# Kernel tuning notes

Measured on AMD Instinct MI355X. Metric: run time of the kernel, lower is better.

The kernel has to match this reference:

```python
import jax, jax.numpy as jnp
import numpy as np

EPS = 1e-5


def _bn(h, gamma, beta):
    # BatchNorm1d in training mode: batch statistics over node dim
    mu = h.mean(axis=0)
    var = h.var(axis=0)
    return gamma * (h - mu) * jax.lax.rsqrt(var + EPS) + beta


def _rgcn_layer(x, src, dst, etype, W, Wloop, b, n_dst):
    # Relation-specific gather-transform-scatter (DGL RelGraphConv, sum agg,
    # self-loop + bias, no regularizer).
    x_src = x[src]                                   # [E, in] gather
    num_rels = W.shape[0]
    m = jnp.zeros((x_src.shape[0], W.shape[2]), x.dtype)
    for r in range(num_rels):                        # small fixed relation count
        m = m + jnp.where((etype == r)[:, None], x_src @ W[r], 0.0)
    agg = jax.ops.segment_sum(m, dst, num_segments=n_dst)  # scatter-add to dst
    # DGL block convention: dst nodes are the prefix of src nodes
    return agg + x[:n_dst] @ Wloop + b


def setup_inputs() -> dict:
    key = jax.random.key(0)
    ks = jax.random.split(key, 16)
    N_SRC, N_DST0, N_DST1 = 200000, 50000, 10000
    E0, E1, R, H, C = 800000, 160000, 5, 256, 153
    s = 1.0 / np.sqrt(H)
    inp = {
        "x": jax.random.normal(ks[0], (N_SRC, H), jnp.float32),
        "src0": jax.random.randint(ks[1], (E0,), 0, N_SRC, jnp.int32),
        "dst0": jax.random.randint(ks[2], (E0,), 0, N_DST0, jnp.int32),
        "etype0": jax.random.randint(ks[3], (E0,), 0, R, jnp.int32),
        "src1": jax.random.randint(ks[4], (E1,), 0, N_DST0, jnp.int32),
        "dst1": jax.random.randint(ks[5], (E1,), 0, N_DST1, jnp.int32),
        "etype1": jax.random.randint(ks[6], (E1,), 0, R, jnp.int32),
        "n_dst0": N_DST0,
        "n_dst1": N_DST1,
        "W0": jax.random.normal(ks[7], (R, H, H), jnp.float32) * s,
        "Wl0": jax.random.normal(ks[8], (H, H), jnp.float32) * s,
        "b0": jnp.zeros((H,), jnp.float32),
        "g0": jnp.ones((H,), jnp.float32),
        "be0": jnp.zeros((H,), jnp.float32),
        "W1": jax.random.normal(ks[9], (R, H, H), jnp.float32) * s,
        "Wl1": jax.random.normal(ks[10], (H, H), jnp.float32) * s,
        "b1": jnp.zeros((H,), jnp.float32),
        "g1": jnp.ones((H,), jnp.float32),
        "be1": jnp.zeros((H,), jnp.float32),
        "Wm1": jax.random.normal(ks[11], (H, H), jnp.float32) * s,
        "bm1": jnp.zeros((H,), jnp.float32),
        "gm": jnp.ones((H,), jnp.float32),
        "bem": jnp.zeros((H,), jnp.float32),
        "Wm2": jax.random.normal(ks[12], (H, C), jnp.float32) * s,
        "bm2": jnp.zeros((C,), jnp.float32),
    }
    return inp


def reference(x, src0, dst0, etype0, src1, dst1, etype1, n_dst0, n_dst1,
              W0, Wl0, b0, g0, be0, W1, Wl1, b1, g1, be1,
              Wm1, bm1, gm, bem, Wm2, bm2):
    # layer 0
    h = _rgcn_layer(x, src0, dst0, etype0, W0, Wl0, b0, n_dst0)
    h = jax.nn.elu(_bn(h, g0, be0))
    # layer 1
    h = _rgcn_layer(h, src1, dst1, etype1, W1, Wl1, b1, n_dst1)
    h = jax.nn.elu(_bn(h, g1, be1))
    # MLP head (dropout is identity in eval)
    h = jax.nn.relu(_bn(h @ Wm1 + bm1, gm, bem))
    return h @ Wm2 + bm2
```

## Files before the change

### kernel.cpp

```cpp
#include <hip/hip_runtime.h>
#include <hip/hip_bf16.h>


#define HD   256
#define EPS  1e-5f
#define NREL 5
#define ND0  50000
#define ND1  10000

typedef unsigned short ushort_t;
using f32x4  = __attribute__((ext_vector_type(4))) float;
using short8 = __attribute__((ext_vector_type(8))) short;

__device__ __forceinline__ ushort_t f2b(float f) {
    union { float f; unsigned u; } x; x.f = f;
    unsigned r = x.u + 0x7FFF + ((x.u >> 16) & 1);
    return (ushort_t)(r >> 16);
}
__device__ __forceinline__ float b2f(ushort_t h) {
    union { unsigned u; float f; } x; x.u = ((unsigned)h) << 16;
    return x.f;
}

#define GLOAD_LDS16(gp, lp)                                                     \
    __builtin_amdgcn_global_load_lds(                                           \
        (const __attribute__((address_space(1))) unsigned int*)(gp),            \
        (__attribute__((address_space(3))) unsigned int*)(lp), 16, 0, 0)

struct WconvArgs {
    const float* src[14];
    ushort_t*    dst[14];
    int          N[14];
};
__global__ void wconv_all_kernel(WconvArgs a) {
    int mat = blockIdx.x >> 8;
    int id = (blockIdx.x & 255) * 256 + threadIdx.x;
    int n = id >> 8, k = id & 255;
    int N = a.N[mat];
    float v = (n < N) ? a.src[mat][(size_t)k * N + n] : 0.f;
    a.dst[mat][id] = f2b(v);
}

__global__ void xconv_kernel(const float* __restrict__ x, ushort_t* __restrict__ xb,
                             int n4) {
    int id = blockIdx.x * 256 + threadIdx.x;
    if (id >= n4) return;
    float4 v = ((const float4*)x)[id];
    ushort4 o; o.x = f2b(v.x); o.y = f2b(v.y); o.z = f2b(v.z); o.w = f2b(v.w);
    ((ushort4*)xb)[id] = o;
}

__global__ void count2_kernel(const int* __restrict__ d0, const int* __restrict__ e0, int E0,
                              const int* __restrict__ d1, const int* __restrict__ e1, int E1,
                              int* __restrict__ cnt, int* __restrict__ pos) {
    int e = blockIdx.x * 256 + threadIdx.x;
    if (e < E0) {
        pos[e] = atomicAdd(&cnt[e0[e] * ND0 + d0[e]], 1);
    } else if (e < E0 + E1) {
        int i = e - E0;
        pos[e] = atomicAdd(&cnt[NREL * ND0 + e1[i] * ND1 + d1[i]], 1);
    }
}

__global__ void scan_block_kernel(const int* __restrict__ in, int* __restrict__ out,
                                  int* __restrict__ bsum, int nb) {
    __shared__ int ts[256];
    int tid = threadIdx.x;
    int base = blockIdx.x * 1024 + tid * 4;
    int v0 = (base + 0 < nb) ? in[base + 0] : 0;
    int v1 = (base + 1 < nb) ? in[base + 1] : 0;
    int v2 = (base + 2 < nb) ? in[base + 2] : 0;
    int v3 = (base + 3 < nb) ? in[base + 3] : 0;
    int tsum = v0 + v1 + v2 + v3;
    ts[tid] = tsum;
    __syncthreads();
    for (int d = 1; d < 256; d <<= 1) {
        int t = (tid >= d) ? ts[tid - d] : 0;
        __syncthreads();
        ts[tid] += t;
        __syncthreads();
    }
    int excl = ts[tid] - tsum;
    if (base + 0 < nb) out[base + 0] = excl;
    if (base + 1 < nb) out[base + 1] = excl + v0;
    if (base + 2 < nb) out[base + 2] = excl + v0 + v1;
    if (base + 3 < nb) out[base + 3] = excl + v0 + v1 + v2;
    if (tid == 255 && bsum) bsum[blockIdx.x] = ts[255];
}

__global__ void scan_add_kernel(int* __restrict__ out, const int* __restrict__ bsum, int nb) {
    int i = blockIdx.x * 256 + threadIdx.x;
    if (i < nb) out[i] += bsum[i >> 10];
}

__global__ void fill2_kernel(const int* __restrict__ s0, const int* __restrict__ d0,
                             const int* __restrict__ e0, int E0,
                             const int* __restrict__ s1, const int* __restrict__ d1,
                             const int* __restrict__ e1, int E1,
                             const int* __restrict__ pos, const int* __restrict__ off,
                             int* __restrict__ ssrc) {
    int e = blockIdx.x * 256 + threadIdx.x;
    if (e < E0) {
        ssrc[off[e0[e] * ND0 + d0[e]] + pos[e]] = s0[e];
    } else if (e < E0 + E1) {
        int i = e - E0;
        ssrc[off[NREL * ND0 + e1[i] * ND1 + d1[i]] + pos[e]] = s1[i];
    }
}

__device__ __forceinline__ void bnelu_acc(ushort4 v, const float4& scv, const float4& shv,
                                          float& a0, float& a1, float& a2, float& a3) {
    float f0 = fmaf(b2f(v.x), scv.x, shv.x);
    float f1 = fmaf(b2f(v.y), scv.y, shv.y);
    float f2 = fmaf(b2f(v.z), scv.z, shv.z);
    float f3 = fmaf(b2f(v.w), scv.w, shv.w);
    a0 += f0 > 0.f ? f0 : expm1f(f0);
    a1 += f1 > 0.f ? f1 : expm1f(f1);
    a2 += f2 > 0.f ? f2 : expm1f(f2);
    a3 += f3 > 0.f ? f3 : expm1f(f3);
}

__global__ void gather_kernel(const ushort_t* __restrict__ feat, const int* __restrict__ ssrc,
                              const int* __restrict__ cnt, const int* __restrict__ off,
                              int nbuckets, ushort_t* __restrict__ out,
                              const float* __restrict__ sc, const float* __restrict__ sh) {
    int wave = (blockIdx.x * 256 + threadIdx.x) >> 6;
    int lane = threadIdx.x & 63;
    if (wave >= nbuckets) return;
    int deg = cnt[wave], s = off[wave];
    float a0 = 0, a1 = 0, a2 = 0, a3 = 0;
    if (sc) {
        float4 scv = ((const float4*)sc)[lane];
        float4 shv = ((const float4*)sh)[lane];
        int j = 0;
        for (; j + 4 <= deg; j += 4) {
            int r0 = ssrc[s + j + 0], r1 = ssrc[s + j + 1];
            int r2 = ssrc[s + j + 2], r3 = ssrc[s + j + 3];
            ushort4 v0 = ((const ushort4*)(feat + (size_t)r0 * HD))[lane];
            ushort4 v1 = ((const ushort4*)(feat + (size_t)r1 * HD))[lane];
            ushort4 v2 = ((const ushort4*)(feat + (size_t)r2 * HD))[lane];
            ushort4 v3 = ((const ushort4*)(feat + (size_t)r3 * HD))[lane];
            bnelu_acc(v0, scv, shv, a0, a1, a2, a3);
            bnelu_acc(v1, scv, shv, a0, a1, a2, a3);
            bnelu_acc(v2, scv, shv, a0, a1, a2, a3);
            bnelu_acc(v3, scv, shv, a0, a1, a2, a3);
        }
        for (; j < deg; j++) {
            ushort4 v = ((const ushort4*)(feat + (size_t)ssrc[s + j] * HD))[lane];
            bnelu_acc(v, scv, shv, a0, a1, a2, a3);
        }
    } else {
        int j = 0;
        for (; j + 4 <= deg; j += 4) {
            int r0 = ssrc[s + j + 0], r1 = ssrc[s + j + 1];
            int r2 = ssrc[s + j + 2], r3 = ssrc[s + j + 3];
            ushort4 v0 = ((const ushort4*)(feat + (size_t)r0 * HD))[lane];
            ushort4 v1 = ((const ushort4*)(feat + (size_t)r1 * HD))[lane];
            ushort4 v2 = ((const ushort4*)(feat + (size_t)r2 * HD))[lane];
            ushort4 v3 = ((const ushort4*)(feat + (size_t)r3 * HD))[lane];
            a0 += b2f(v0.x) + b2f(v1.x) + b2f(v2.x) + b2f(v3.x);
            a1 += b2f(v0.y) + b2f(v1.y) + b2f(v2.y) + b2f(v3.y);
            a2 += b2f(v0.z) + b2f(v1.z) + b2f(v2.z) + b2f(v3.z);
            a3 += b2f(v0.w) + b2f(v1.w) + b2f(v2.w) + b2f(v3.w);
        }
        for (; j < deg; j++) {
            ushort4 v = ((const ushort4*)(feat + (size_t)ssrc[s + j] * HD))[lane];
            a0 += b2f(v.x); a1 += b2f(v.y); a2 += b2f(v.z); a3 += b2f(v.w);
        }
    }
    ushort4 o; o.x = f2b(a0); o.y = f2b(a1); o.z = f2b(a2); o.w = f2b(a3);
    ((ushort4*)(out + (size_t)wave * HD))[lane] = o;
}

__global__ void bnprep_kernel(const float* __restrict__ sums, const float* __restrict__ g,
                              const float* __restrict__ be, float invM,
                              float* __restrict__ sc, float* __restrict__ sh) {
    int c = threadIdx.x;
    float mu = sums[c] * invM;
    float var = sums[HD + c] * invM - mu * mu;
    float s = g[c] * rsqrtf(var + EPS);
    sc[c] = s; sh[c] = be[c] - mu * s;
}

__global__ void bnact_kernel(const ushort_t* __restrict__ in, ushort_t* __restrict__ out,
                             const float* __restrict__ sc, const float* __restrict__ sh,
                             int act, int n64) {
    int id = blockIdx.x * 256 + threadIdx.x;
    if (id >= n64) return;
    int c4 = id & 63;
    ushort4 v = ((const ushort4*)in)[id];
    float4 scv = ((const float4*)sc)[c4];
    float4 shv = ((const float4*)sh)[c4];
    float f0 = fmaf(b2f(v.x), scv.x, shv.x);
    float f1 = fmaf(b2f(v.y), scv.y, shv.y);
    float f2 = fmaf(b2f(v.z), scv.z, shv.z);
    float f3 = fmaf(b2f(v.w), scv.w, shv.w);
    if (act == 2) {
        f0 = fmaxf(f0, 0.f); f1 = fmaxf(f1, 0.f);
        f2 = fmaxf(f2, 0.f); f3 = fmaxf(f3, 0.f);
    } else {
        f0 = f0 > 0.f ? f0 : expm1f(f0);
        f1 = f1 > 0.f ? f1 : expm1f(f1);
        f2 = f2 > 0.f ? f2 : expm1f(f2);
        f3 = f3 > 0.f ? f3 : expm1f(f3);
    }
    ushort4 o; o.x = f2b(f0); o.y = f2b(f1); o.z = f2b(f2); o.w = f2b(f3);
    ((ushort4*)out)[id] = o;
}

struct Seg {
    const ushort_t* A;
    const ushort_t* B;
};
struct GemmArgs {
    Seg seg[6];
    int nseg;
    const float* bias;
    float* stats;
    ushort_t* Cb;
    float* Cf;
    int M, N;
};

__launch_bounds__(512, 2)
__global__ void gemm256_kernel(GemmArgs g) {
    __shared__ __align__(1024) ushort_t As[4][8192];
    __shared__ __align__(1024) ushort_t Bs[4][8192];
    int tid = threadIdx.x;
    int w = tid >> 6, lane = tid & 63;
    int rq = lane >> 4, ci = lane & 15;
    int wm = (w >> 2) * 128, wn = (w & 3) * 64;
    int bm = blockIdx.y * 256;
    f32x4 acc[8][4] = {};
    int NT = (g.nseg * HD) >> 5;

    auto stage = [&](int b, int t) {
        int k = t << 5;
        int si = k >> 8, kl = k & 255;
        const ushort_t* Ap = g.seg[si].A;
        const ushort_t* Bp = g.seg[si].B;
        int ft = w * 2;
        GLOAD_LDS16(Ap + (size_t)(bm + ft * 16 + ci) * HD + kl + rq * 8,
                    &As[b][ft * 512 + lane * 8]);
        GLOAD_LDS16(Ap + (size_t)(bm + ft * 16 + 16 + ci) * HD + kl + rq * 8,
                    &As[b][(ft + 1) * 512 + lane * 8]);
        GLOAD_LDS16(Bp + (size_t)(ft * 16 + ci) * HD + kl + rq * 8,
                    &Bs[b][ft * 512 + lane * 8]);
        GLOAD_LDS16(Bp + (size_t)(ft * 16 + 16 + ci) * HD + kl + rq * 8,
                    &Bs[b][(ft + 1) * 512 + lane * 8]);
    };

    stage(0, 0);
    if (NT > 1) stage(1, 1);
    if (NT > 2) stage(2, 2);
    for (int t = 0; t < NT; t++) {
        int buf = t & 3;
        int rem = NT - t;
        if (rem >= 3)      asm volatile("s_waitcnt vmcnt(8)" ::: "memory");
        else if (rem == 2) asm volatile("s_waitcnt vmcnt(4)" ::: "memory");
        else               asm volatile("s_waitcnt vmcnt(0)" ::: "memory");
        __builtin_amdgcn_s_barrier();
        if (t + 3 < NT) stage((t + 3) & 3, t + 3);
        short8 bfr[4];
#pragma unroll
        for (int ni = 0; ni < 4; ni++)
            bfr[ni] = *(const short8*)&Bs[buf][((wn >> 4) + ni) * 512 + lane * 8];
#pragma unroll
        for (int mi = 0; mi < 8; mi++) {
            short8 afr = *(const short8*)&As[buf][((wm >> 4) + mi) * 512 + lane * 8];
#pragma unroll
            for (int ni = 0; ni < 4; ni++)
                acc[mi][ni] = __builtin_amdgcn_mfma_f32_16x16x32_bf16(
                    afr, bfr[ni], acc[mi][ni], 0, 0, 0);
        }
    }

#pragma unroll
    for (int ni = 0; ni < 4; ni++) {
        int col = wn + ni * 16 + ci;
        float bv = (col < g.N) ? g.bias[col] : 0.f;
#pragma unroll
        for (int mi = 0; mi < 8; mi++)
#pragma unroll
            for (int reg = 0; reg < 4; reg++) acc[mi][ni][reg] += bv;
    }
    if (g.stats) {
#pragma unroll
        for (int ni = 0; ni < 4; ni++) {
            float s = 0.f, s2 = 0.f;
#pragma unroll
            for (int mi = 0; mi < 8; mi++)
#pragma unroll
                for (int reg = 0; reg < 4; reg++) {
                    int row = bm + wm + mi * 16 + rq * 4 + reg;
                    if (row < g.M) { float v = acc[mi][ni][reg]; s += v; s2 += v * v; }
                }
            s  += __shfl_xor(s, 16);  s  += __shfl_xor(s, 32);
            s2 += __shfl_xor(s2, 16); s2 += __shfl_xor(s2, 32);
            if (rq == 0) {
                int col = wn + ni * 16 + ci;
                atomicAdd(&g.stats[col], s);
                atomicAdd(&g.stats[HD + col], s2);
            }
        }
    }
#pragma unroll
    for (int mi = 0; mi < 8; mi++)
#pragma unroll
        for (int ni = 0; ni < 4; ni++)
#pragma unroll
            for (int reg = 0; reg < 4; reg++) {
                int row = bm + wm + mi * 16 + rq * 4 + reg;
                int col = wn + ni * 16 + ci;
                if (row < g.M && col < g.N) {
                    float v = acc[mi][ni][reg];
                    if (g.Cb) g.Cb[(size_t)row * HD + col] = f2b(v);
                    else      g.Cf[(size_t)row * g.N + col] = v;
                }
            }
}

extern "C" void kernel_launch(void* const* d_in, const int* in_sizes, int n_in,
                              void* d_out, int out_size, void* d_ws, size_t ws_size,
                              hipStream_t stream) {
    const float* x   = (const float*)d_in[0];
    const int* src0  = (const int*)d_in[1];
    const int* dst0  = (const int*)d_in[2];
    const int* et0   = (const int*)d_in[3];
    const int* src1  = (const int*)d_in[4];
    const int* dst1  = (const int*)d_in[5];
    const int* et1   = (const int*)d_in[6];
    const float* W0  = (const float*)d_in[9];
    const float* Wl0 = (const float*)d_in[10];
    const float* b0  = (const float*)d_in[11];
    const float* g0  = (const float*)d_in[12];
    const float* be0 = (const float*)d_in[13];
    const float* W1  = (const float*)d_in[14];
    const float* Wl1 = (const float*)d_in[15];
    const float* b1  = (const float*)d_in[16];
    const float* g1  = (const float*)d_in[17];
    const float* be1 = (const float*)d_in[18];
    const float* Wm1 = (const float*)d_in[19];
    const float* bm1 = (const float*)d_in[20];
    const float* gm  = (const float*)d_in[21];
    const float* bem = (const float*)d_in[22];
    const float* Wm2 = (const float*)d_in[23];
    const float* bm2 = (const float*)d_in[24];

    const int E0 = in_sizes[1];
    const int E1 = in_sizes[4];
    const int NOUT = in_sizes[24];
    const int NSRC = in_sizes[0] / HD;
    const int NBKT = NREL * ND0 + NREL * ND1;

    char* p = (char*)d_ws;
    ushort_t* Wt = (ushort_t*)p;  p += (size_t)14 * 65536 * 2;
    float* st    = (float*)p;     p += 1536 * 4;
    float* bnp   = (float*)p;     p += 6 * 256 * 4;
    int* cnt     = (int*)p;       p += (size_t)NBKT * 4;
    int* off     = (int*)p;       p += (size_t)NBKT * 4;
    int* bsum    = (int*)p;       p += 1024 * 4;
    int* pos     = (int*)p;       p += (size_t)(E0 + E1) * 4;
    int* ssrc    = (int*)p;       p += (size_t)(E0 + E1) * 4;
    ushort_t* xb  = (ushort_t*)p; p += (size_t)NSRC * HD * 2;
    ushort_t* S0  = (ushort_t*)p; p += (size_t)(NREL * ND0 + 512) * HD * 2;
    ushort_t* S1  = (ushort_t*)p; p += (size_t)(NREL * ND1 + 512) * HD * 2;
    ushort_t* h0b = (ushort_t*)p; p += (size_t)(ND0 + 512) * HD * 2;
    ushort_t* h1b = (ushort_t*)p; p += (size_t)(ND1 + 512) * HD * 2;
    ushort_t* mb  = (ushort_t*)p; p += (size_t)(ND1 + 512) * HD * 2;
    ushort_t* h0a = (ushort_t*)p; p += (size_t)(ND1 + 512) * HD * 2;
    ushort_t* h1a = (ushort_t*)p; p += (size_t)(ND1 + 512) * HD * 2;
    ushort_t* ma  = (ushort_t*)p; p += (size_t)(ND1 + 512) * HD * 2;

    float* st0 = st, *st1 = st + 512, *stm = st + 1024;
    float* sc0 = bnp, *sh0 = bnp + 256, *sc1 = bnp + 512, *sh1 = bnp + 768;
    float* scm = bnp + 1024, *shm = bnp + 1280;

    ushort_t* W0t  = Wt;
    ushort_t* Wl0t = Wt + 5 * 65536;
    ushort_t* W1t  = Wt + 6 * 65536;
    ushort_t* Wl1t = Wt + 11 * 65536;
    ushort_t* Wm1t = Wt + 12 * 65536;
    ushort_t* Wm2t = Wt + 13 * 65536;

    {
        WconvArgs wa;
        for (int r = 0; r < NREL; r++) { wa.src[r] = W0 + (size_t)r * 65536; wa.dst[r] = W0t + (size_t)r * 65536; wa.N[r] = 256; }
        wa.src[5] = Wl0; wa.dst[5] = Wl0t; wa.N[5] = 256;
        for (int r = 0; r < NREL; r++) { wa.src[6 + r] = W1 + (size_t)r * 65536; wa.dst[6 + r] = W1t + (size_t)r * 65536; wa.N[6 + r] = 256; }
        wa.src[11] = Wl1; wa.dst[11] = Wl1t; wa.N[11] = 256;
        wa.src[12] = Wm1; wa.dst[12] = Wm1t; wa.N[12] = 256;
        wa.src[13] = Wm2; wa.dst[13] = Wm2t; wa.N[13] = NOUT;
        wconv_all_kernel<<<14 * 256, 256, 0, stream>>>(wa);
    }
    xconv_kernel<<<(NSRC * 64 + 255) / 256, 256, 0, stream>>>(x, xb, NSRC * 64);
    hipMemsetAsync(st, 0, 1536 * sizeof(float), stream);
    hipMemsetAsync(cnt, 0, (size_t)NBKT * sizeof(int), stream);

    int ET = E0 + E1;
    count2_kernel<<<(ET + 255) / 256, 256, 0, stream>>>(dst0, et0, E0, dst1, et1, E1, cnt, pos);
    int nsb = (NBKT + 1023) / 1024;
    scan_block_kernel<<<nsb, 256, 0, stream>>>(cnt, off, bsum, NBKT);
    scan_block_kernel<<<1, 256, 0, stream>>>(bsum, bsum, nullptr, nsb);
    scan_add_kernel<<<(NBKT + 255) / 256, 256, 0, stream>>>(off, bsum, NBKT);
    fill2_kernel<<<(ET + 255) / 256, 256, 0, stream>>>(src0, dst0, et0, E0, src1, dst1, et1, E1, pos, off, ssrc);

    gather_kernel<<<(NREL * ND0 * 64) / 256, 256, 0, stream>>>(
        xb, ssrc, cnt, off, NREL * ND0, S0, nullptr, nullptr);
    {
        GemmArgs ga = {};
        for (int s = 0; s < NREL; s++)
            ga.seg[s] = { S0 + (size_t)s * ND0 * HD, W0t + (size_t)s * 65536 };
        ga.seg[5] = { xb, Wl0t };
        ga.nseg = 6; ga.bias = b0; ga.stats = st0;
        ga.Cb = h0b; ga.Cf = nullptr; ga.M = ND0; ga.N = HD;
        gemm256_kernel<<<dim3(1, (ND0 + 255) / 256), 512, 0, stream>>>(ga);
    }
    bnprep_kernel<<<1, 256, 0, stream>>>(st0, g0, be0, 1.f / ND0, sc0, sh0);

    bnact_kernel<<<((ND1 + 240) * 64 + 255) / 256, 256, 0, stream>>>(
        h0b, h0a, sc0, sh0, 1, (ND1 + 240) * 64);
    gather_kernel<<<(NREL * ND1 * 64) / 256, 256, 0, stream>>>(
        h0b, ssrc, cnt + NREL * ND0, off + NREL * ND0, NREL * ND1, S1, sc0, sh0);
    {
        GemmArgs ga = {};
        for (int s = 0; s < NREL; s++)
            ga.seg[s] = { S1 + (size_t)s * ND1 * HD, W1t + (size_t)s * 65536 };
        ga.seg[5] = { h0a, Wl1t };
        ga.nseg = 6; ga.bias = b1; ga.stats = st1;
        ga.Cb = h1b; ga.Cf = nullptr; ga.M = ND1; ga.N = HD;
        gemm256_kernel<<<dim3(1, (ND1 + 255) / 256), 512, 0, stream>>>(ga);
    }
    bnprep_kernel<<<1, 256, 0, stream>>>(st1, g1, be1, 1.f / ND1, sc1, sh1);

    bnact_kernel<<<((ND1 + 240) * 64 + 255) / 256, 256, 0, stream>>>(
        h1b, h1a, sc1, sh1, 1, (ND1 + 240) * 64);
    {
        GemmArgs ga = {};
        ga.seg[0] = { h1a, Wm1t };
        ga.nseg = 1; ga.bias = bm1; ga.stats = stm;
        ga.Cb = mb; ga.Cf = nullptr; ga.M = ND1; ga.N = HD;
        gemm256_kernel<<<dim3(1, (ND1 + 255) / 256), 512, 0, stream>>>(ga);
    }
    bnprep_kernel<<<1, 256, 0, stream>>>(stm, gm, bem, 1.f / ND1, scm, shm);
    bnact_kernel<<<((ND1 + 240) * 64 + 255) / 256, 256, 0, stream>>>(
        mb, ma, scm, shm, 2, (ND1 + 240) * 64);
    {
        GemmArgs ga = {};
        ga.seg[0] = { ma, Wm2t };
        ga.nseg = 1; ga.bias = bm2; ga.stats = nullptr;
        ga.Cb = nullptr; ga.Cf = (float*)d_out; ga.M = ND1; ga.N = NOUT;
        gemm256_kernel<<<dim3(1, (ND1 + 255) / 256), 512, 0, stream>>>(ga);
    }
}
```

Measured before the change: 808.4 us.

## Switch GEMM to 128x128 tiles with 256 threads and simplify gather unrolling

Replaces the 256x256, 512-thread GEMM with a 128x128, 256-thread tile that also splits N across blockIdx.x. The grid therefore has more blocks to spread across the CUs, and each wave holds fewer accumulators. The gather kernel loses its 4-way unroll: the BN+ELU path now processes one neighbor per iteration and the plain path processes two, which cuts register use but reduces memory-level parallelism. Padding for bnact is enlarged to cover 128-row tiles.

```diff
diff --git a/kernel.cpp b/kernel.cpp
--- a/kernel.cpp
+++ b/kernel.cpp
@@ -108,18 +108,6 @@
     }
 }
 
-__device__ __forceinline__ void bnelu_acc(ushort4 v, const float4& scv, const float4& shv,
-                                          float& a0, float& a1, float& a2, float& a3) {
-    float f0 = fmaf(b2f(v.x), scv.x, shv.x);
-    float f1 = fmaf(b2f(v.y), scv.y, shv.y);
-    float f2 = fmaf(b2f(v.z), scv.z, shv.z);
-    float f3 = fmaf(b2f(v.w), scv.w, shv.w);
-    a0 += f0 > 0.f ? f0 : expm1f(f0);
-    a1 += f1 > 0.f ? f1 : expm1f(f1);
-    a2 += f2 > 0.f ? f2 : expm1f(f2);
-    a3 += f3 > 0.f ? f3 : expm1f(f3);
-}
-
 __global__ void gather_kernel(const ushort_t* __restrict__ feat, const int* __restrict__ ssrc,
                               const int* __restrict__ cnt, const int* __restrict__ off,
                               int nbuckets, ushort_t* __restrict__ out,
@@ -128,42 +116,31 @@
     int lane = threadIdx.x & 63;
     if (wave >= nbuckets) return;
     int deg = cnt[wave], s = off[wave];
+    float4 scv = {0, 0, 0, 0}, shv = {0, 0, 0, 0};
+    if (sc) { scv = ((const float4*)sc)[lane]; shv = ((const float4*)sh)[lane]; }
     float a0 = 0, a1 = 0, a2 = 0, a3 = 0;
     if (sc) {
-        float4 scv = ((const float4*)sc)[lane];
-        float4 shv = ((const float4*)sh)[lane];
-        int j = 0;
-        for (; j + 4 <= deg; j += 4) {
-            int r0 = ssrc[s + j + 0], r1 = ssrc[s + j + 1];
-            int r2 = ssrc[s + j + 2], r3 = ssrc[s + j + 3];
-            ushort4 v0 = ((const ushort4*)(feat + (size_t)r0 * HD))[lane];
-            ushort4 v1 = ((const ushort4*)(feat + (size_t)r1 * HD))[lane];
-            ushort4 v2 = ((const ushort4*)(feat + (size_t)r2 * HD))[lane];
-            ushort4 v3 = ((const ushort4*)(feat + (size_t)r3 * HD))[lane];
-            bnelu_acc(v0, scv, shv, a0, a1, a2, a3);
-            bnelu_acc(v1, scv, shv, a0, a1, a2, a3);
-            bnelu_acc(v2, scv, shv, a0, a1, a2, a3);
-            bnelu_acc(v3, scv, shv, a0, a1, a2, a3);
-        }
-        for (; j < deg; j++) {
+        for (int j = 0; j < deg; j++) {
             ushort4 v = ((const ushort4*)(feat + (size_t)ssrc[s + j] * HD))[lane];
-            bnelu_acc(v, scv, shv, a0, a1, a2, a3);
+            float f0 = fmaf(b2f(v.x), scv.x, shv.x);
+            float f1 = fmaf(b2f(v.y), scv.y, shv.y);
+            float f2 = fmaf(b2f(v.z), scv.z, shv.z);
+            float f3 = fmaf(b2f(v.w), scv.w, shv.w);
+            a0 += f0 > 0.f ? f0 : expm1f(f0);
+            a1 += f1 > 0.f ? f1 : expm1f(f1);
+            a2 += f2 > 0.f ? f2 : expm1f(f2);
+            a3 += f3 > 0.f ? f3 : expm1f(f3);
         }
     } else {
         int j = 0;
-        for (; j + 4 <= deg; j += 4) {
-            int r0 = ssrc[s + j + 0], r1 = ssrc[s + j + 1];
-            int r2 = ssrc[s + j + 2], r3 = ssrc[s + j + 3];
+        for (; j + 2 <= deg; j += 2) {
+            int r0 = ssrc[s + j], r1 = ssrc[s + j + 1];
             ushort4 v0 = ((const ushort4*)(feat + (size_t)r0 * HD))[lane];
             ushort4 v1 = ((const ushort4*)(feat + (size_t)r1 * HD))[lane];
-            ushort4 v2 = ((const ushort4*)(feat + (size_t)r2 * HD))[lane];
-            ushort4 v3 = ((const ushort4*)(feat + (size_t)r3 * HD))[lane];
-            a0 += b2f(v0.x) + b2f(v1.x) + b2f(v2.x) + b2f(v3.x);
-            a1 += b2f(v0.y) + b2f(v1.y) + b2f(v2.y) + b2f(v3.y);
-            a2 += b2f(v0.z) + b2f(v1.z) + b2f(v2.z) + b2f(v3.z);
-            a3 += b2f(v0.w) + b2f(v1.w) + b2f(v2.w) + b2f(v3.w);
+            a0 += b2f(v0.x) + b2f(v1.x); a1 += b2f(v0.y) + b2f(v1.y);
+            a2 += b2f(v0.z) + b2f(v1.z); a3 += b2f(v0.w) + b2f(v1.w);
         }
-        for (; j < deg; j++) {
+        if (j < deg) {
             ushort4 v = ((const ushort4*)(feat + (size_t)ssrc[s + j] * HD))[lane];
             a0 += b2f(v.x); a1 += b2f(v.y); a2 += b2f(v.z); a3 += b2f(v.w);
         }
@@ -222,16 +199,17 @@
     int M, N;
 };
 
-__launch_bounds__(512, 2)
-__global__ void gemm256_kernel(GemmArgs g) {
-    __shared__ __align__(1024) ushort_t As[4][8192];
-    __shared__ __align__(1024) ushort_t Bs[4][8192];
+__launch_bounds__(256, 2)
+__global__ void gemm_ring_kernel(GemmArgs g) {
+    __shared__ __align__(1024) ushort_t As[4][4096];
+    __shared__ __align__(1024) ushort_t Bs[4][4096];
     int tid = threadIdx.x;
     int w = tid >> 6, lane = tid & 63;
     int rq = lane >> 4, ci = lane & 15;
-    int wm = (w >> 2) * 128, wn = (w & 3) * 64;
-    int bm = blockIdx.y * 256;
-    f32x4 acc[8][4] = {};
+    int wm = (w >> 1) * 64, wn = (w & 1) * 64;
+    int wmf = wm >> 4, wnf = wn >> 4;
+    int bm = blockIdx.y * 128, bn = blockIdx.x * 128;
+    f32x4 acc[4][4] = {};
     int NT = (g.nseg * HD) >> 5;
 
     auto stage = [&](int b, int t) {
@@ -242,11 +220,11 @@
         int ft = w * 2;
         GLOAD_LDS16(Ap + (size_t)(bm + ft * 16 + ci) * HD + kl + rq * 8,
                     &As[b][ft * 512 + lane * 8]);
-        GLOAD_LDS16(Ap + (size_t)(bm + ft * 16 + 16 + ci) * HD + kl + rq * 8,
+        GLOAD_LDS16(Ap + (size_t)(bm + (ft + 1) * 16 + ci) * HD + kl + rq * 8,
                     &As[b][(ft + 1) * 512 + lane * 8]);
-        GLOAD_LDS16(Bp + (size_t)(ft * 16 + ci) * HD + kl + rq * 8,
+        GLOAD_LDS16(Bp + (size_t)(bn + ft * 16 + ci) * HD + kl + rq * 8,
                     &Bs[b][ft * 512 + lane * 8]);
-        GLOAD_LDS16(Bp + (size_t)(ft * 16 + 16 + ci) * HD + kl + rq * 8,
+        GLOAD_LDS16(Bp + (size_t)(bn + (ft + 1) * 16 + ci) * HD + kl + rq * 8,
                     &Bs[b][(ft + 1) * 512 + lane * 8]);
     };
 
@@ -260,27 +238,29 @@
         else if (rem == 2) asm volatile("s_waitcnt vmcnt(4)" ::: "memory");
         else               asm volatile("s_waitcnt vmcnt(0)" ::: "memory");
         __builtin_amdgcn_s_barrier();
+        __builtin_amdgcn_sched_barrier(0);
         if (t + 3 < NT) stage((t + 3) & 3, t + 3);
-        short8 bfr[4];
+        short8 a[4], b[4];
 #pragma unroll
         for (int ni = 0; ni < 4; ni++)
-            bfr[ni] = *(const short8*)&Bs[buf][((wn >> 4) + ni) * 512 + lane * 8];
-#pragma unroll
-        for (int mi = 0; mi < 8; mi++) {
-            short8 afr = *(const short8*)&As[buf][((wm >> 4) + mi) * 512 + lane * 8];
+            b[ni] = *(const short8*)&Bs[buf][(wnf + ni) * 512 + lane * 8];
+#pragma unroll
+        for (int mi = 0; mi < 4; mi++)
+            a[mi] = *(const short8*)&As[buf][(wmf + mi) * 512 + lane * 8];
+#pragma unroll
+        for (int mi = 0; mi < 4; mi++)
 #pragma unroll
             for (int ni = 0; ni < 4; ni++)
                 acc[mi][ni] = __builtin_amdgcn_mfma_f32_16x16x32_bf16(
-                    afr, bfr[ni], acc[mi][ni], 0, 0, 0);
-        }
+                    a[mi], b[ni], acc[mi][ni], 0, 0, 0);
     }
 
 #pragma unroll
     for (int ni = 0; ni < 4; ni++) {
-        int col = wn + ni * 16 + ci;
+        int col = bn + wn + ni * 16 + ci;
         float bv = (col < g.N) ? g.bias[col] : 0.f;
 #pragma unroll
-        for (int mi = 0; mi < 8; mi++)
+        for (int mi = 0; mi < 4; mi++)
 #pragma unroll
             for (int reg = 0; reg < 4; reg++) acc[mi][ni][reg] += bv;
     }
@@ -289,7 +269,7 @@
         for (int ni = 0; ni < 4; ni++) {
             float s = 0.f, s2 = 0.f;
 #pragma unroll
-            for (int mi = 0; mi < 8; mi++)
+            for (int mi = 0; mi < 4; mi++)
 #pragma unroll
                 for (int reg = 0; reg < 4; reg++) {
                     int row = bm + wm + mi * 16 + rq * 4 + reg;
@@ -298,20 +278,20 @@
             s  += __shfl_xor(s, 16);  s  += __shfl_xor(s, 32);
             s2 += __shfl_xor(s2, 16); s2 += __shfl_xor(s2, 32);
             if (rq == 0) {
-                int col = wn + ni * 16 + ci;
+                int col = bn + wn + ni * 16 + ci;
                 atomicAdd(&g.stats[col], s);
                 atomicAdd(&g.stats[HD + col], s2);
             }
         }
     }
 #pragma unroll
-    for (int mi = 0; mi < 8; mi++)
+    for (int mi = 0; mi < 4; mi++)
 #pragma unroll
         for (int ni = 0; ni < 4; ni++)
 #pragma unroll
             for (int reg = 0; reg < 4; reg++) {
                 int row = bm + wm + mi * 16 + rq * 4 + reg;
-                int col = wn + ni * 16 + ci;
+                int col = bn + wn + ni * 16 + ci;
                 if (row < g.M && col < g.N) {
                     float v = acc[mi][ni][reg];
                     if (g.Cb) g.Cb[(size_t)row * HD + col] = f2b(v);
@@ -414,12 +394,12 @@
         ga.seg[5] = { xb, Wl0t };
         ga.nseg = 6; ga.bias = b0; ga.stats = st0;
         ga.Cb = h0b; ga.Cf = nullptr; ga.M = ND0; ga.N = HD;
-        gemm256_kernel<<<dim3(1, (ND0 + 255) / 256), 512, 0, stream>>>(ga);
+        gemm_ring_kernel<<<dim3(2, (ND0 + 127) / 128), 256, 0, stream>>>(ga);
     }
     bnprep_kernel<<<1, 256, 0, stream>>>(st0, g0, be0, 1.f / ND0, sc0, sh0);
 
-    bnact_kernel<<<((ND1 + 240) * 64 + 255) / 256, 256, 0, stream>>>(
-        h0b, h0a, sc0, sh0, 1, (ND1 + 240) * 64);
+    bnact_kernel<<<((ND1 + 512) * 64 + 255) / 256, 256, 0, stream>>>(
+        h0b, h0a, sc0, sh0, 1, (ND1 + 512) * 64);
     gather_kernel<<<(NREL * ND1 * 64) / 256, 256, 0, stream>>>(
         h0b, ssrc, cnt + NREL * ND0, off + NREL * ND0, NREL * ND1, S1, sc0, sh0);
     {
@@ -429,27 +409,27 @@
         ga.seg[5] = { h0a, Wl1t };
         ga.nseg = 6; ga.bias = b1; ga.stats = st1;
         ga.Cb = h1b; ga.Cf = nullptr; ga.M = ND1; ga.N = HD;
-        gemm256_kernel<<<dim3(1, (ND1 + 255) / 256), 512, 0, stream>>>(ga);
+        gemm_ring_kernel<<<dim3(2, (ND1 + 127) / 128), 256, 0, stream>>>(ga);
     }
     bnprep_kernel<<<1, 256, 0, stream>>>(st1, g1, be1, 1.f / ND1, sc1, sh1);
 
-    bnact_kernel<<<((ND1 + 240) * 64 + 255) / 256, 256, 0, stream>>>(
-        h1b, h1a, sc1, sh1, 1, (ND1 + 240) * 64);
+    bnact_kernel<<<((ND1 + 512) * 64 + 255) / 256, 256, 0, stream>>>(
+        h1b, h1a, sc1, sh1, 1, (ND1 + 512) * 64);
     {
         GemmArgs ga = {};
         ga.seg[0] = { h1a, Wm1t };
         ga.nseg = 1; ga.bias = bm1; ga.stats = stm;
         ga.Cb = mb; ga.Cf = nullptr; ga.M = ND1; ga.N = HD;
-        gemm256_kernel<<<dim3(1, (ND1 + 255) / 256), 512, 0, stream>>>(ga);
+        gemm_ring_kernel<<<dim3(2, (ND1 + 127) / 128), 256, 0, stream>>>(ga);
     }
     bnprep_kernel<<<1, 256, 0, stream>>>(stm, gm, bem, 1.f / ND1, scm, shm);
-    bnact_kernel<<<((ND1 + 240) * 64 + 255) / 256, 256, 0, stream>>>(
-        mb, ma, scm, shm, 2, (ND1 + 240) * 64);
+    bnact_kernel<<<((ND1 + 512) * 64 + 255) / 256, 256, 0, stream>>>(
+        mb, ma, scm, shm, 2, (ND1 + 512) * 64);
     {
         GemmArgs ga = {};
         ga.seg[0] = { ma, Wm2t };
         ga.nseg = 1; ga.bias = bm2; ga.stats = nullptr;
         ga.Cb = nullptr; ga.Cf = (float*)d_out; ga.M = ND1; ga.N = NOUT;
-        gemm256_kernel<<<dim3(1, (ND1 + 255) / 256), 512, 0, stream>>>(ga);
-    }
-}
+        gemm_ring_kernel<<<dim3((NOUT + 127) / 128, (ND1 + 127) / 128), 256, 0, stream>>>(ga);
+    }
+}
```

Result: faster. 785.7 us (-2.8%).
